# Kernel tuning notes

Hardware: AMD Instinct MI355X
Metric: run time of the kernel (lower is better)

Reference implementation:

```python
import jax, jax.numpy as jnp
import numpy as np

B, T, I, H, O = 512, 2048, 4, 100, 1


def setup_inputs() -> dict:
    key = jax.random.key(0)
    k1, k2, k3, k4 = jax.random.split(key, 4)
    s_ih = 1.0 / np.sqrt(H)
    return {
        "x": jax.random.normal(k1, (B, T, I), dtype=jnp.float32),
        "W_ih": jax.random.uniform(k2, (H, I), minval=-s_ih, maxval=s_ih, dtype=jnp.float32),
        "W_hh": jax.random.uniform(k3, (H, H), minval=-s_ih, maxval=s_ih, dtype=jnp.float32),
        "W_fc": jax.random.uniform(k4, (O, H), minval=-s_ih, maxval=s_ih, dtype=jnp.float32),
        "b_fc": jnp.zeros((O,), dtype=jnp.float32),
    }


def reference(x, W_ih, W_hh, W_fc, b_fc):
    # Precompute input projections for all timesteps: [T, B, H]
    xp = jnp.einsum("bti,hi->tbh", x, W_ih)
    h0 = jnp.zeros((x.shape[0], W_hh.shape[0]), dtype=x.dtype)

    def step(h, xp_t):
        h_new = jnp.tanh(xp_t + h @ W_hh.T)
        return h_new, h_new

    _, hs = jax.lax.scan(step, h0, xp)          # hs: [T, B, H]
    hs = jnp.swapaxes(hs, 0, 1)                 # [B, T, H]
    out = jnp.einsum("bth,oh->bto", hs, W_fc) + b_fc  # [B, T, O]
    return out
```

## Files before the change

kernel.cpp:

```cpp
#include <hip/hip_runtime.h>


#define BB 512
#define TT 2048
#define II 4
#define HH 100
#define HP 116
#define CHUNK 64
#define NCH (TT / CHUNK)

__device__ __forceinline__ float rlf(float v, int l) {
    return __int_as_float(__builtin_amdgcn_readlane(__float_as_int(v), l));
}

__global__ __launch_bounds__(128, 1) void crnn_kernel(
    const float* __restrict__ x,
    const float* __restrict__ W_ih,
    const float* __restrict__ W_hh,
    const float* __restrict__ W_fc,
    const float* __restrict__ b_fc,
    float* __restrict__ out)
{
    __shared__ float xs[TT * II];
    __shared__ float hh[CHUNK * HP];
    __shared__ float wfcs[HP];
    __shared__ float pt[2][CHUNK];

    const int tid  = threadIdx.x;
    const int b    = blockIdx.x;
    const int lane = tid & 63;
    const int w    = tid >> 6;
    const int j    = tid;
    const int jj   = (j < HH) ? j : HH - 1;
    const bool act = (j < HH);

    const float4* xg = reinterpret_cast<const float4*>(x + (size_t)b * TT * II);
    float4* xl = reinterpret_cast<float4*>(xs);
#pragma unroll
    for (int it = 0; it < (TT * II / 4) / 128; ++it)
        xl[it * 128 + tid] = xg[it * 128 + tid];

    float4 wih = reinterpret_cast<const float4*>(W_ih)[jj];
    float wr[HH];
    const float4* wrow = reinterpret_cast<const float4*>(W_hh + jj * HH);
#pragma unroll
    for (int k4 = 0; k4 < HH / 4; ++k4) {
        float4 v = wrow[k4];
        wr[4 * k4 + 0] = v.x; wr[4 * k4 + 1] = v.y;
        wr[4 * k4 + 2] = v.z; wr[4 * k4 + 3] = v.w;
    }
    if (tid < HP) wfcs[tid] = (tid < HH) ? W_fc[tid] : 0.f;
    const float bias = b_fc[0];
    for (int i = tid; i < CHUNK * (HP - HH); i += 128) {
        int r = i / (HP - HH), p = i % (HP - HH);
        hh[r * HP + HH + p] = 0.f;
    }
    __syncthreads();

    const int voff = w ? lane : (64 + (lane < 36 ? lane : 35));

    float vh = 0.f;
    float vo = 0.f;
    float* outb = out + (size_t)b * TT;

    for (int c = 0; c < NCH; ++c) {
        const float4* xs4 = reinterpret_cast<const float4*>(xs) + c * CHUNK;
        for (int t = 0; t < CHUNK; ++t) {
            float4 xv = xs4[t];
            float a0 = wih.x * xv.x;
            float a1 = wih.y * xv.y;
            float a2 = wih.z * xv.z;
            float a3 = wih.w * xv.w;
            if (w == 0) {
#pragma unroll
                for (int k = 0; k < 64; k += 4) {
                    a0 = fmaf(wr[k + 0], rlf(vh, k + 0), a0);
                    a1 = fmaf(wr[k + 1], rlf(vh, k + 1), a1);
                    a2 = fmaf(wr[k + 2], rlf(vh, k + 2), a2);
                    a3 = fmaf(wr[k + 3], rlf(vh, k + 3), a3);
                }
#pragma unroll
                for (int k = 64; k < 100; k += 4) {
                    a0 = fmaf(wr[k + 0], rlf(vo, k - 64 + 0), a0);
                    a1 = fmaf(wr[k + 1], rlf(vo, k - 64 + 1), a1);
                    a2 = fmaf(wr[k + 2], rlf(vo, k - 64 + 2), a2);
                    a3 = fmaf(wr[k + 3], rlf(vo, k - 64 + 3), a3);
                }
            } else {
#pragma unroll
                for (int k = 64; k < 100; k += 4) {
                    a0 = fmaf(wr[k + 0], rlf(vh, k - 64 + 0), a0);
                    a1 = fmaf(wr[k + 1], rlf(vh, k - 64 + 1), a1);
                    a2 = fmaf(wr[k + 2], rlf(vh, k - 64 + 2), a2);
                    a3 = fmaf(wr[k + 3], rlf(vh, k - 64 + 3), a3);
                }
#pragma unroll
                for (int k = 0; k < 64; k += 4) {
                    a0 = fmaf(wr[k + 0], rlf(vo, k + 0), a0);
                    a1 = fmaf(wr[k + 1], rlf(vo, k + 1), a1);
                    a2 = fmaf(wr[k + 2], rlf(vo, k + 2), a2);
                    a3 = fmaf(wr[k + 3], rlf(vo, k + 3), a3);
                }
            }
            float acc = (a0 + a1) + (a2 + a3);
            float e   = __expf(2.f * acc);
            float hn  = 1.f - 2.f * __builtin_amdgcn_rcpf(e + 1.f);
            vh = hn;
            float* rowW = hh + t * HP;
            if (act) rowW[j] = hn;
            __syncthreads();
            vo = rowW[voff];
        }

        const int tl = tid & (CHUNK - 1);
        const int kh = tid >> 6;
        const int k0 = kh * 52;
        const float4* wf4 = reinterpret_cast<const float4*>(wfcs + k0);
        const float4* hr  = reinterpret_cast<const float4*>(hh + tl * HP + k0);
        float csum = 0.f;
#pragma unroll
        for (int i = 0; i < 13; ++i) {
            float4 hvv = hr[i];
            float4 wv  = wf4[i];
            csum = fmaf(hvv.x, wv.x, csum);
            csum = fmaf(hvv.y, wv.y, csum);
            csum = fmaf(hvv.z, wv.z, csum);
            csum = fmaf(hvv.w, wv.w, csum);
        }
        pt[kh][tl] = csum;
        __syncthreads();
        if (tid < CHUNK) outb[c * CHUNK + tid] = (pt[0][tid] + pt[1][tid]) + bias;
    }
}

extern "C" void kernel_launch(void* const* d_in, const int* in_sizes, int n_in,
                              void* d_out, int out_size, void* d_ws, size_t ws_size,
                              hipStream_t stream) {
    const float* x    = (const float*)d_in[0];
    const float* W_ih = (const float*)d_in[1];
    const float* W_hh = (const float*)d_in[2];
    const float* W_fc = (const float*)d_in[3];
    const float* b_fc = (const float*)d_in[4];
    float* out = (float*)d_out;
    crnn_kernel<<<BB, 128, 0, stream>>>(x, W_ih, W_hh, W_fc, b_fc, out);
}
```

Measured before the change: 962.6 us.

## Move step barrier mid-recurrence and software-pipeline readlane broadcasts

Each wave now first accumulates the part of the recurrent matvec that uses its own wave's hidden values. It then hits the barrier and reads the other wave's previous-step values from shared memory, so local FMA work overlaps the barrier wait instead of preceding a barrier at the end of the step. Readlane broadcasts are prefetched eight at a time into two alternating register sets to hide their latency behind the FMAs. The shared row pitch shrinks and the whole history buffer is zeroed so the previous-row read at step zero is valid. The cost is more live registers and a more intricate ordering of writes and reads across the ring of rows.

After: 1.110 ms. 1.15x slower.

```diff
diff --git a/kernel.cpp b/kernel.cpp
--- a/kernel.cpp
+++ b/kernel.cpp
@@ -5,13 +5,27 @@
 #define TT 2048
 #define II 4
 #define HH 100
-#define HP 116
+#define HP 108
 #define CHUNK 64
 #define NCH (TT / CHUNK)
 
 __device__ __forceinline__ float rlf(float v, int l) {
     return __int_as_float(__builtin_amdgcn_readlane(__float_as_int(v), l));
 }
+
+#define PF8(B, SRC, L) \
+    B##0 = rlf(SRC, (L)+0); B##1 = rlf(SRC, (L)+1); B##2 = rlf(SRC, (L)+2); B##3 = rlf(SRC, (L)+3); \
+    B##4 = rlf(SRC, (L)+4); B##5 = rlf(SRC, (L)+5); B##6 = rlf(SRC, (L)+6); B##7 = rlf(SRC, (L)+7);
+#define PF4(B, SRC, L) \
+    B##0 = rlf(SRC, (L)+0); B##1 = rlf(SRC, (L)+1); B##2 = rlf(SRC, (L)+2); B##3 = rlf(SRC, (L)+3);
+#define FM8(B, K) \
+    a0 = fmaf(wr[(K)+0], B##0, a0); a1 = fmaf(wr[(K)+1], B##1, a1); \
+    a2 = fmaf(wr[(K)+2], B##2, a2); a3 = fmaf(wr[(K)+3], B##3, a3); \
+    a0 = fmaf(wr[(K)+4], B##4, a0); a1 = fmaf(wr[(K)+5], B##5, a1); \
+    a2 = fmaf(wr[(K)+6], B##6, a2); a3 = fmaf(wr[(K)+7], B##7, a3);
+#define FM4(B, K) \
+    a0 = fmaf(wr[(K)+0], B##0, a0); a1 = fmaf(wr[(K)+1], B##1, a1); \
+    a2 = fmaf(wr[(K)+2], B##2, a2); a3 = fmaf(wr[(K)+3], B##3, a3);
 
 __global__ __launch_bounds__(128, 1) void crnn_kernel(
     const float* __restrict__ x,
@@ -51,67 +65,75 @@
     }
     if (tid < HP) wfcs[tid] = (tid < HH) ? W_fc[tid] : 0.f;
     const float bias = b_fc[0];
-    for (int i = tid; i < CHUNK * (HP - HH); i += 128) {
-        int r = i / (HP - HH), p = i % (HP - HH);
-        hh[r * HP + HH + p] = 0.f;
-    }
+    for (int i = tid; i < CHUNK * HP; i += 128) hh[i] = 0.f;
     __syncthreads();
 
     const int voff = w ? lane : (64 + (lane < 36 ? lane : 35));
 
     float vh = 0.f;
-    float vo = 0.f;
     float* outb = out + (size_t)b * TT;
 
     for (int c = 0; c < NCH; ++c) {
         const float4* xs4 = reinterpret_cast<const float4*>(xs) + c * CHUNK;
-        for (int t = 0; t < CHUNK; ++t) {
-            float4 xv = xs4[t];
+#pragma unroll 1
+        for (int s = 0; s < CHUNK; ++s) {
+            const float* rowPrev = hh + (((s + CHUNK - 1) & (CHUNK - 1)) * HP);
+            float4 xv = xs4[s];
             float a0 = wih.x * xv.x;
             float a1 = wih.y * xv.y;
             float a2 = wih.z * xv.z;
             float a3 = wih.w * xv.w;
+            float p0,p1,p2,p3,p4,p5,p6,p7;
+            float q0,q1,q2,q3,q4,q5,q6,q7;
+            float vo;
+
             if (w == 0) {
-#pragma unroll
-                for (int k = 0; k < 64; k += 4) {
-                    a0 = fmaf(wr[k + 0], rlf(vh, k + 0), a0);
-                    a1 = fmaf(wr[k + 1], rlf(vh, k + 1), a1);
-                    a2 = fmaf(wr[k + 2], rlf(vh, k + 2), a2);
-                    a3 = fmaf(wr[k + 3], rlf(vh, k + 3), a3);
-                }
-#pragma unroll
-                for (int k = 64; k < 100; k += 4) {
-                    a0 = fmaf(wr[k + 0], rlf(vo, k - 64 + 0), a0);
-                    a1 = fmaf(wr[k + 1], rlf(vo, k - 64 + 1), a1);
-                    a2 = fmaf(wr[k + 2], rlf(vo, k - 64 + 2), a2);
-                    a3 = fmaf(wr[k + 3], rlf(vo, k - 64 + 3), a3);
-                }
+                PF8(p, vh, 0)
+                PF8(q, vh, 8)   FM8(p, 0)
+                PF8(p, vh, 16)  FM8(q, 8)
+                PF8(q, vh, 24)  FM8(p, 16)
             } else {
-#pragma unroll
-                for (int k = 64; k < 100; k += 4) {
-                    a0 = fmaf(wr[k + 0], rlf(vh, k - 64 + 0), a0);
-                    a1 = fmaf(wr[k + 1], rlf(vh, k - 64 + 1), a1);
-                    a2 = fmaf(wr[k + 2], rlf(vh, k - 64 + 2), a2);
-                    a3 = fmaf(wr[k + 3], rlf(vh, k - 64 + 3), a3);
-                }
-#pragma unroll
-                for (int k = 0; k < 64; k += 4) {
-                    a0 = fmaf(wr[k + 0], rlf(vo, k + 0), a0);
-                    a1 = fmaf(wr[k + 1], rlf(vo, k + 1), a1);
-                    a2 = fmaf(wr[k + 2], rlf(vo, k + 2), a2);
-                    a3 = fmaf(wr[k + 3], rlf(vo, k + 3), a3);
-                }
+                PF8(p, vh, 0)
+                PF8(q, vh, 8)   FM8(p, 64)
             }
+
+            __syncthreads();
+            vo = rowPrev[voff];
+
+            if (w == 0) {
+                PF8(p, vh, 32)  FM8(q, 24)
+                PF8(q, vh, 40)  FM8(p, 32)
+                PF8(p, vh, 48)  FM8(q, 40)
+                PF8(q, vh, 56)  FM8(p, 48)
+                PF8(p, vo, 0)   FM8(q, 56)
+                PF8(q, vo, 8)   FM8(p, 64)
+                PF8(p, vo, 16)  FM8(q, 72)
+                PF8(q, vo, 24)  FM8(p, 80)
+                PF4(p, vo, 32)  FM8(q, 88)
+                FM4(p, 96)
+            } else {
+                PF8(p, vh, 16)  FM8(q, 72)
+                PF8(q, vh, 24)  FM8(p, 80)
+                PF4(p, vh, 32)  FM8(q, 88)
+                PF8(q, vo, 0)   FM4(p, 96)
+                PF8(p, vo, 8)   FM8(q, 0)
+                PF8(q, vo, 16)  FM8(p, 8)
+                PF8(p, vo, 24)  FM8(q, 16)
+                PF8(q, vo, 32)  FM8(p, 24)
+                PF8(p, vo, 40)  FM8(q, 32)
+                PF8(q, vo, 48)  FM8(p, 40)
+                PF8(p, vo, 56)  FM8(q, 48)
+                FM8(p, 56)
+            }
+
             float acc = (a0 + a1) + (a2 + a3);
             float e   = __expf(2.f * acc);
             float hn  = 1.f - 2.f * __builtin_amdgcn_rcpf(e + 1.f);
             vh = hn;
-            float* rowW = hh + t * HP;
-            if (act) rowW[j] = hn;
-            __syncthreads();
-            vo = rowW[voff];
+            if (act) hh[s * HP + j] = hn;
         }
 
+        __syncthreads();
         const int tl = tid & (CHUNK - 1);
         const int kh = tid >> 6;
         const int k0 = kh * 52;
```

## Split recurrent matvec along K across two wavefronts with partial-sum exchange

Applied to the files above, without the earlier changes.

Each wavefront now handles 50 of the 100 reduction columns for two output rows per lane (rows lane and 64+lane), instead of each thread owning a full row. The two waves swap partial sums through double-buffered shared memory and both compute tanh, so each wave holds the full hidden state in registers and can broadcast it with readlane. This balances the FMA work between the waves and removes the shared-memory round trip that previously fed the other wave's hidden values. The cost is duplicated tanh and exp work and a dependency on the other wave's partial sum every step.

After: 1.031 ms. 1.07x slower.

```diff
diff --git a/kernel.cpp b/kernel.cpp
--- a/kernel.cpp
+++ b/kernel.cpp
@@ -5,7 +5,8 @@
 #define TT 2048
 #define II 4
 #define HH 100
-#define HP 116
+#define KH 50
+#define HP 108
 #define CHUNK 64
 #define NCH (TT / CHUNK)
 
@@ -21,18 +22,18 @@
     const float* __restrict__ b_fc,
     float* __restrict__ out)
 {
-    __shared__ float xs[TT * II];
-    __shared__ float hh[CHUNK * HP];
-    __shared__ float wfcs[HP];
-    __shared__ float pt[2][CHUNK];
+    __shared__ float  xs[TT * II];
+    __shared__ float  hh[CHUNK * HP];
+    __shared__ float  wfcs[HP];
+    __shared__ float2 pw[2][2][64];
+    __shared__ float  pt[2][CHUNK];
 
     const int tid  = threadIdx.x;
     const int b    = blockIdx.x;
     const int lane = tid & 63;
     const int w    = tid >> 6;
-    const int j    = tid;
-    const int jj   = (j < HH) ? j : HH - 1;
-    const bool act = (j < HH);
+    const int rA   = lane;
+    const int rB   = (lane < HH - 64) ? (64 + lane) : (HH - 1);
 
     const float4* xg = reinterpret_cast<const float4*>(x + (size_t)b * TT * II);
     float4* xl = reinterpret_cast<float4*>(xs);
@@ -40,15 +41,19 @@
     for (int it = 0; it < (TT * II / 4) / 128; ++it)
         xl[it * 128 + tid] = xg[it * 128 + tid];
 
-    float4 wih = reinterpret_cast<const float4*>(W_ih)[jj];
-    float wr[HH];
-    const float4* wrow = reinterpret_cast<const float4*>(W_hh + jj * HH);
+    float wA[KH], wB[KH];
+    {
+        const float2* pa = reinterpret_cast<const float2*>(W_hh + rA * HH + w * KH);
+        const float2* pb = reinterpret_cast<const float2*>(W_hh + rB * HH + w * KH);
 #pragma unroll
-    for (int k4 = 0; k4 < HH / 4; ++k4) {
-        float4 v = wrow[k4];
-        wr[4 * k4 + 0] = v.x; wr[4 * k4 + 1] = v.y;
-        wr[4 * k4 + 2] = v.z; wr[4 * k4 + 3] = v.w;
+        for (int i = 0; i < KH / 2; ++i) {
+            float2 va = pa[i], vb = pb[i];
+            wA[2 * i] = va.x; wA[2 * i + 1] = va.y;
+            wB[2 * i] = vb.x; wB[2 * i + 1] = vb.y;
+        }
     }
+    float4 wihA = reinterpret_cast<const float4*>(W_ih)[rA];
+    float4 wihB = reinterpret_cast<const float4*>(W_ih)[rB];
     if (tid < HP) wfcs[tid] = (tid < HH) ? W_fc[tid] : 0.f;
     const float bias = b_fc[0];
     for (int i = tid; i < CHUNK * (HP - HH); i += 128) {
@@ -57,61 +62,92 @@
     }
     __syncthreads();
 
-    const int voff = w ? lane : (64 + (lane < 36 ? lane : 35));
-
-    float vh = 0.f;
-    float vo = 0.f;
+    float vh  = 0.f;
+    float vh2 = 0.f;
     float* outb = out + (size_t)b * TT;
+    const float4* xs4 = reinterpret_cast<const float4*>(xs);
 
     for (int c = 0; c < NCH; ++c) {
-        const float4* xs4 = reinterpret_cast<const float4*>(xs) + c * CHUNK;
-        for (int t = 0; t < CHUNK; ++t) {
-            float4 xv = xs4[t];
-            float a0 = wih.x * xv.x;
-            float a1 = wih.y * xv.y;
-            float a2 = wih.z * xv.z;
-            float a3 = wih.w * xv.w;
+#pragma unroll 1
+        for (int s = 0; s < CHUNK; ++s) {
+            float a0 = 0.f, a1 = 0.f, a2 = 0.f, a3 = 0.f;
+            float b0 = 0.f, b1 = 0.f, b2 = 0.f, b3 = 0.f;
+
             if (w == 0) {
+                float4 xv = xs4[c * CHUNK + s];
+                a0 = wihA.x * xv.x; a1 = wihA.y * xv.y;
+                a2 = wihA.z * xv.z; a3 = wihA.w * xv.w;
+                b0 = wihB.x * xv.x; b1 = wihB.y * xv.y;
+                b2 = wihB.z * xv.z; b3 = wihB.w * xv.w;
 #pragma unroll
-                for (int k = 0; k < 64; k += 4) {
-                    a0 = fmaf(wr[k + 0], rlf(vh, k + 0), a0);
-                    a1 = fmaf(wr[k + 1], rlf(vh, k + 1), a1);
-                    a2 = fmaf(wr[k + 2], rlf(vh, k + 2), a2);
-                    a3 = fmaf(wr[k + 3], rlf(vh, k + 3), a3);
+                for (int i = 0; i < 48; i += 4) {
+                    float h0 = rlf(vh, i + 0), h1 = rlf(vh, i + 1);
+                    float h2 = rlf(vh, i + 2), h3 = rlf(vh, i + 3);
+                    a0 = fmaf(wA[i + 0], h0, a0);  b0 = fmaf(wB[i + 0], h0, b0);
+                    a1 = fmaf(wA[i + 1], h1, a1);  b1 = fmaf(wB[i + 1], h1, b1);
+                    a2 = fmaf(wA[i + 2], h2, a2);  b2 = fmaf(wB[i + 2], h2, b2);
+                    a3 = fmaf(wA[i + 3], h3, a3);  b3 = fmaf(wB[i + 3], h3, b3);
                 }
-#pragma unroll
-                for (int k = 64; k < 100; k += 4) {
-                    a0 = fmaf(wr[k + 0], rlf(vo, k - 64 + 0), a0);
-                    a1 = fmaf(wr[k + 1], rlf(vo, k - 64 + 1), a1);
-                    a2 = fmaf(wr[k + 2], rlf(vo, k - 64 + 2), a2);
-                    a3 = fmaf(wr[k + 3], rlf(vo, k - 64 + 3), a3);
+                {
+                    float h0 = rlf(vh, 48), h1 = rlf(vh, 49);
+                    a0 = fmaf(wA[48], h0, a0);  b0 = fmaf(wB[48], h0, b0);
+                    a1 = fmaf(wA[49], h1, a1);  b1 = fmaf(wB[49], h1, b1);
                 }
             } else {
 #pragma unroll
-                for (int k = 64; k < 100; k += 4) {
-                    a0 = fmaf(wr[k + 0], rlf(vh, k - 64 + 0), a0);
-                    a1 = fmaf(wr[k + 1], rlf(vh, k - 64 + 1), a1);
-                    a2 = fmaf(wr[k + 2], rlf(vh, k - 64 + 2), a2);
-                    a3 = fmaf(wr[k + 3], rlf(vh, k - 64 + 3), a3);
+                for (int i = 0; i < 12; i += 4) {
+                    float h0 = rlf(vh, 50 + i), h1 = rlf(vh, 51 + i);
+                    float h2 = rlf(vh, 52 + i), h3 = rlf(vh, 53 + i);
+                    a0 = fmaf(wA[i + 0], h0, a0);  b0 = fmaf(wB[i + 0], h0, b0);
+                    a1 = fmaf(wA[i + 1], h1, a1);  b1 = fmaf(wB[i + 1], h1, b1);
+                    a2 = fmaf(wA[i + 2], h2, a2);  b2 = fmaf(wB[i + 2], h2, b2);
+                    a3 = fmaf(wA[i + 3], h3, a3);  b3 = fmaf(wB[i + 3], h3, b3);
+                }
+                {
+                    float h0 = rlf(vh, 62), h1 = rlf(vh, 63);
+                    a0 = fmaf(wA[12], h0, a0);  b0 = fmaf(wB[12], h0, b0);
+                    a1 = fmaf(wA[13], h1, a1);  b1 = fmaf(wB[13], h1, b1);
                 }
 #pragma unroll
-                for (int k = 0; k < 64; k += 4) {
-                    a0 = fmaf(wr[k + 0], rlf(vo, k + 0), a0);
-                    a1 = fmaf(wr[k + 1], rlf(vo, k + 1), a1);
-                    a2 = fmaf(wr[k + 2], rlf(vo, k + 2), a2);
-                    a3 = fmaf(wr[k + 3], rlf(vo, k + 3), a3);
+                for (int i = 14; i < 46; i += 4) {
+                    float h0 = rlf(vh2, i - 14), h1 = rlf(vh2, i - 13);
+                    float h2 = rlf(vh2, i - 12), h3 = rlf(vh2, i - 11);
+                    a0 = fmaf(wA[i + 0], h0, a0);  b0 = fmaf(wB[i + 0], h0, b0);
+                    a1 = fmaf(wA[i + 1], h1, a1);  b1 = fmaf(wB[i + 1], h1, b1);
+                    a2 = fmaf(wA[i + 2], h2, a2);  b2 = fmaf(wB[i + 2], h2, b2);
+                    a3 = fmaf(wA[i + 3], h3, a3);  b3 = fmaf(wB[i + 3], h3, b3);
+                }
+                {
+                    float h0 = rlf(vh2, 32), h1 = rlf(vh2, 33);
+                    float h2 = rlf(vh2, 34), h3 = rlf(vh2, 35);
+                    a0 = fmaf(wA[46], h0, a0);  b0 = fmaf(wB[46], h0, b0);
+                    a1 = fmaf(wA[47], h1, a1);  b1 = fmaf(wB[47], h1, b1);
+                    a2 = fmaf(wA[48], h2, a2);  b2 = fmaf(wB[48], h2, b2);
+                    a3 = fmaf(wA[49], h3, a3);  b3 = fmaf(wB[49], h3, b3);
                 }
             }
-            float acc = (a0 + a1) + (a2 + a3);
-            float e   = __expf(2.f * acc);
-            float hn  = 1.f - 2.f * __builtin_amdgcn_rcpf(e + 1.f);
-            vh = hn;
-            float* rowW = hh + t * HP;
-            if (act) rowW[j] = hn;
+
+            float accA = (a0 + a1) + (a2 + a3);
+            float accB = (b0 + b1) + (b2 + b3);
+
+            pw[s & 1][w][lane] = make_float2(accA, accB);
             __syncthreads();
-            vo = rowW[voff];
+            float2 po = pw[s & 1][w ^ 1][lane];
+            float sA = accA + po.x;
+            float sB = accB + po.y;
+
+            float eA = __expf(2.f * sA);
+            float eB = __expf(2.f * sB);
+            vh  = 1.f - 2.f * __builtin_amdgcn_rcpf(eA + 1.f);
+            vh2 = 1.f - 2.f * __builtin_amdgcn_rcpf(eB + 1.f);
+
+            if (w == 0) {
+                hh[s * HP + lane] = vh;
+                if (lane < HH - 64) hh[s * HP + 64 + lane] = vh2;
+            }
         }
 
+        __syncthreads();
         const int tl = tid & (CHUNK - 1);
         const int kh = tid >> 6;
         const int k0 = kh * 52;
```
